# Kernel tuning notes

Measured on AMD Instinct MI355X. Metric: run time of the kernel, lower is better.

Reference implementation:

```python
import jax, jax.numpy as jnp
import numpy as np

NEG_SLOPE = 0.2  # PyG GATConv default negative_slope
N_NODES = 40000
N_EDGES = 640000
IN_DIM = 128
SAT_DIM = 64
HID = 128
OUT_DIM = 54


def gat_conv(x, edge_index, W, a_src, a_dst, bias):
    """PyG GATConv with heads=1, concat=True, add_self_loops=True."""
    n = x.shape[0]
    loops = jnp.arange(n, dtype=edge_index.dtype)
    src = jnp.concatenate([edge_index[0], loops])  # message sources j
    dst = jnp.concatenate([edge_index[1], loops])  # message targets i
    h = x @ W.T                                    # [N, C]
    alpha_s = h @ a_src                            # [N]
    alpha_d = h @ a_dst                            # [N]
    e = jax.nn.leaky_relu(alpha_s[src] + alpha_d[dst], NEG_SLOPE)  # [E]
    # segment softmax over incoming edges of each dst node (self-loops guarantee non-empty segments)
    m = jax.ops.segment_max(e, dst, num_segments=n)
    e = jnp.exp(e - m[dst])
    denom = jax.ops.segment_sum(e, dst, num_segments=n)
    alpha = e / (denom[dst] + 1e-16)
    out = jax.ops.segment_sum(alpha[:, None] * h[src], dst, num_segments=n)
    return out + bias


def setup_inputs() -> dict:
    key = jax.random.key(0)
    ks = jax.random.split(key, 16)
    s = lambda d: 1.0 / np.sqrt(d)
    inp = {
        "x": jax.random.normal(ks[0], (N_NODES, IN_DIM), jnp.float32),
        "edge_index": jax.random.randint(ks[1], (2, N_EDGES), 0, N_NODES, jnp.int32),
        "sat_W": jax.random.normal(ks[2], (HID, SAT_DIM), jnp.float32) * s(SAT_DIM),
        "sat_b": jnp.zeros((HID,), jnp.float32),
        "neigh_W": jax.random.normal(ks[3], (HID, IN_DIM - SAT_DIM), jnp.float32) * s(IN_DIM - SAT_DIM),
        "neigh_b": jnp.zeros((HID,), jnp.float32),
        "conv1_W": jax.random.normal(ks[4], (HID, HID), jnp.float32) * s(HID),
        "conv1_asrc": jax.random.normal(ks[5], (HID,), jnp.float32) * s(HID),
        "conv1_adst": jax.random.normal(ks[6], (HID,), jnp.float32) * s(HID),
        "conv1_b": jnp.zeros((HID,), jnp.float32),
        "conv2_W": jax.random.normal(ks[7], (HID, HID), jnp.float32) * s(HID),
        "conv2_asrc": jax.random.normal(ks[8], (HID,), jnp.float32) * s(HID),
        "conv2_adst": jax.random.normal(ks[9], (HID,), jnp.float32) * s(HID),
        "conv2_b": jnp.zeros((HID,), jnp.float32),
        "fc1_W": jax.random.normal(ks[10], (HID, HID), jnp.float32) * s(HID),
        "fc1_b": jnp.zeros((HID,), jnp.float32),
        "fc2_W": jax.random.normal(ks[11], (OUT_DIM, HID), jnp.float32) * s(HID),
        "fc2_b": jnp.zeros((OUT_DIM,), jnp.float32),
    }
    return inp


def reference(x, edge_index, sat_W, sat_b, neigh_W, neigh_b,
              conv1_W, conv1_asrc, conv1_adst, conv1_b,
              conv2_W, conv2_asrc, conv2_adst, conv2_b,
              fc1_W, fc1_b, fc2_W, fc2_b):
    sat = jax.nn.relu(x[:, :SAT_DIM] @ sat_W.T + sat_b)
    nei = jax.nn.relu(x[:, SAT_DIM:] @ neigh_W.T + neigh_b)
    h = sat + 0.5 * nei
    h = jax.nn.relu(gat_conv(h, edge_index, conv1_W, conv1_asrc, conv1_adst, conv1_b))
    h = jax.nn.relu(gat_conv(h, edge_index, conv2_W, conv2_asrc, conv2_adst, conv2_b))
    h = jax.nn.relu(h @ fc1_W.T + fc1_b)
    return h @ fc2_W.T + fc2_b
```

## Files before the change

### kernel.cpp

```cpp
#include <hip/hip_runtime.h>


#define N_NODES 40000
#define N_EDGES 640000
#define DIM     128

typedef unsigned short u16;
typedef __attribute__((ext_vector_type(8))) short bf16x8;
typedef __attribute__((ext_vector_type(4))) float f32x4;

#define GLOAD_LDS16(GSRC, LDST)                                                \
    __builtin_amdgcn_global_load_lds(                                          \
        (const __attribute__((address_space(1))) void*)(GSRC),                 \
        (__attribute__((address_space(3))) void*)(LDST), 16, 0, 0)

__device__ __forceinline__ u16 f2bf(float v) {
    unsigned u = __float_as_uint(v);
    u += 0x7FFFu + ((u >> 16) & 1u);
    return (u16)(u >> 16);
}
__device__ __forceinline__ float bf2f(u16 h) { return __uint_as_float(((unsigned)h) << 16); }
__device__ __forceinline__ float rdlane_f(float v, int l) {
    return __uint_as_float(__builtin_amdgcn_readlane(__float_as_uint(v), l));
}

__device__ __forceinline__ int hswz(int row, int col) {
    return row * 128 + ((((col >> 2) ^ (row & 7))) << 2) + (col & 3);
}
__device__ __forceinline__ float4 hread4(const float* hbuf, int row, int k) {
    int b = (k >> 2) ^ (row & 7);
    return *(const float4*)&hbuf[row * 128 + (b << 2)];
}
__device__ __forceinline__ void split8(const float* vv, bf16x8& hi, bf16x8& lo) {
#pragma unroll
    for (int i = 0; i < 8; ++i) {
        u16 h = f2bf(vv[i]);
        hi[i] = (short)h;
        lo[i] = (short)f2bf(vv[i] - bf2f(h));
    }
}

#define MFMA3(ACC, AH, AL, BH, BL)                                             \
    ACC = __builtin_amdgcn_mfma_f32_16x16x32_bf16(AH, BH, ACC, 0, 0, 0);       \
    ACC = __builtin_amdgcn_mfma_f32_16x16x32_bf16(AH, BL, ACC, 0, 0, 0);       \
    ACC = __builtin_amdgcn_mfma_f32_16x16x32_bf16(AL, BH, ACC, 0, 0, 0);

__global__ __launch_bounds__(256) void k_wcvt(
    const float* __restrict__ satW, const float* __restrict__ neiW,
    const float* __restrict__ c1W, const float* __restrict__ c2W,
    const float* __restrict__ f1W, const float* __restrict__ f2W,
    u16* __restrict__ wa, int* __restrict__ deg, int* __restrict__ counter) {
    int gid = (blockIdx.y * gridDim.x + blockIdx.x) * 256 + threadIdx.x;
    if (gid < N_NODES) deg[gid] = 1;
    if (gid == 0) *counter = 0;

    int m = blockIdx.y;
    const float* src; int C, K, Cp; int offH, offL;
    switch (m) {
        case 0: src = satW; C = 128; K = 64;  Cp = 128; offH = 0;      offL = 8192;   break;
        case 1: src = neiW; C = 128; K = 64;  Cp = 128; offH = 16384;  offL = 24576;  break;
        case 2: src = c1W;  C = 128; K = 128; Cp = 128; offH = 32768;  offL = 49152;  break;
        case 3: src = c2W;  C = 128; K = 128; Cp = 128; offH = 65536;  offL = 81920;  break;
        case 4: src = f1W;  C = 128; K = 128; Cp = 128; offH = 98304;  offL = 114688; break;
        default:src = f2W;  C = 54;  K = 128; Cp = 64;  offH = 131072; offL = 139264; break;
    }
    int e = blockIdx.x * 256 + threadIdx.x;
    if (e >= Cp * K) return;
    int c = e / K, k = e - c * K;
    float v = (c < C) ? src[c * K + k] : 0.f;
    u16 h = f2bf(v);
    wa[offH + e] = h;
    wa[offL + e] = f2bf(v - bf2f(h));
}

__global__ void k_deg_count(const int* __restrict__ dst, int* __restrict__ deg) {
    int t = blockIdx.x * 256 + threadIdx.x;
    if (t < N_EDGES) atomicAdd(&deg[dst[t]], 1);
}
__global__ void k_assign(const int* __restrict__ deg, int* __restrict__ counter,
                         int* __restrict__ start, int* __restrict__ cursor,
                         int* __restrict__ csr_src) {
    int i = blockIdx.x * 256 + threadIdx.x;
    if (i >= N_NODES) return;
    int d = deg[i];
    int s = atomicAdd(counter, d);
    start[i] = s;
    csr_src[s] = i;
    cursor[i] = s + 1;
}
__global__ void k_fill_edges(const int* __restrict__ src, const int* __restrict__ dst,
                             int* __restrict__ cursor, int* __restrict__ csr_src) {
    int t = blockIdx.x * 256 + threadIdx.x;
    if (t < N_EDGES) {
        int p = atomicAdd(&cursor[dst[t]], 1);
        csr_src[p] = src[t];
    }
}

template<int CT>
__device__ __forceinline__ void stage_W(u16* Ws, const u16* __restrict__ Wh,
                                        const u16* __restrict__ Wl, int kc, int tid) {
    for (int idx = tid; idx < CT * 2 * 2 * 64; idx += 256) {
        int l = idx & 63;
        int q = idx >> 6;
        int hilo = q & 1;
        int ks = (q >> 1) & 1;
        int ct = q >> 2;
        int c = ct * 16 + (l & 15);
        int k = kc * 64 + ks * 32 + (l >> 4) * 8;
        const u16* Wp = hilo ? Wl : Wh;
        GLOAD_LDS16(Wp + (size_t)c * 128 + k, &Ws[idx * 8]);
    }
}
__device__ __forceinline__ void stage_W64(u16* Ws, const u16* __restrict__ Wh,
                                          const u16* __restrict__ Wl, int tid) {
    for (int idx = tid; idx < 2048; idx += 256) {
        int l = idx & 63;
        int q = idx >> 6;
        int hilo = q & 1;
        int ks = (q >> 1) & 1;
        int ct = q >> 2;
        int c = ct * 16 + (l & 15);
        int k = ks * 32 + (l >> 4) * 8;
        const u16* Wp = hilo ? Wl : Wh;
        GLOAD_LDS16(Wp + (size_t)c * 64 + k, &Ws[idx * 8]);
    }
}

__device__ __forceinline__ void alpha_epi(const f32x4* acc, int lane, int r0,
                                          const float* __restrict__ a_src,
                                          const float* __restrict__ a_dst,
                                          float* __restrict__ as_, float* __restrict__ ad_) {
    float ps[4] = {0, 0, 0, 0}, pd[4] = {0, 0, 0, 0};
#pragma unroll
    for (int ct = 0; ct < 8; ++ct) {
        float asv = a_src[ct * 16 + (lane & 15)];
        float adv = a_dst[ct * 16 + (lane & 15)];
#pragma unroll
        for (int r = 0; r < 4; ++r) {
            ps[r] = fmaf(acc[ct][r], asv, ps[r]);
            pd[r] = fmaf(acc[ct][r], adv, pd[r]);
        }
    }
#pragma unroll
    for (int off = 1; off < 16; off <<= 1) {
#pragma unroll
        for (int r = 0; r < 4; ++r) {
            ps[r] += __shfl_xor(ps[r], off);
            pd[r] += __shfl_xor(pd[r], off);
        }
    }
    if ((lane & 15) == 0) {
#pragma unroll
        for (int r = 0; r < 4; ++r) {
            int row = r0 + (lane >> 4) * 4 + r;
            as_[row] = ps[r];
            ad_[row] = pd[r];
        }
    }
}

__global__ __launch_bounds__(256) void k_enc_conv1(
    const float* __restrict__ x,
    const u16* __restrict__ sH, const u16* __restrict__ sL,
    const u16* __restrict__ nH, const u16* __restrict__ nL,
    const float* __restrict__ satb, const float* __restrict__ neib,
    const u16* __restrict__ Wh, const u16* __restrict__ Wl,
    const float* __restrict__ a_src, const float* __restrict__ a_dst,
    u16* __restrict__ outG, float* __restrict__ as_, float* __restrict__ ad_)
{
    __shared__ u16 Wbuf[16384];
    float* hbuf = (float*)Wbuf;
    const int tid = threadIdx.x, lane = tid & 63, wv = tid >> 6;
    const int r0 = blockIdx.x * 64 + wv * 16;
    const int arow = r0 + (lane & 15);
    const int kb = (lane >> 4) * 8;

    bf16x8 axh[4], axl[4];
#pragma unroll
    for (int s = 0; s < 4; ++s) {
        const float* p = x + (size_t)arow * 128 + s * 32 + kb;
        float4 a = *(const float4*)p;
        float4 b = *(const float4*)(p + 4);
        float vv[8] = {a.x, a.y, a.z, a.w, b.x, b.y, b.z, b.w};
        split8(vv, axh[s], axl[s]);
    }

    f32x4 accS[8], accN[8];
#pragma unroll
    for (int ct = 0; ct < 8; ++ct) { accS[ct] = (f32x4){0,0,0,0}; accN[ct] = (f32x4){0,0,0,0}; }

#pragma unroll
    for (int mat = 0; mat < 2; ++mat) {
        if (mat) __syncthreads();
        stage_W64(Wbuf, mat ? nH : sH, mat ? nL : sL, tid);
        __syncthreads();
#pragma unroll
        for (int ct = 0; ct < 8; ++ct) {
#pragma unroll
            for (int ks = 0; ks < 2; ++ks) {
                int s = mat * 2 + ks;
                int base = (ct * 2 + ks) * 1024;
                bf16x8 bh = *reinterpret_cast<const bf16x8*>(&Wbuf[base + lane * 8]);
                bf16x8 bl = *reinterpret_cast<const bf16x8*>(&Wbuf[base + 512 + lane * 8]);
                f32x4* ac = mat ? &accN[ct] : &accS[ct];
                MFMA3((*ac), axh[s], axl[s], bh, bl);
            }
        }
    }
    __syncthreads();

#pragma unroll
    for (int ct = 0; ct < 8; ++ct) {
        int c = ct * 16 + (lane & 15);
        float bs = satb[c], bn = neib[c];
#pragma unroll
        for (int r = 0; r < 4; ++r) {
            int rl = wv * 16 + (lane >> 4) * 4 + r;
            float v = fmaxf(accS[ct][r] + bs, 0.f) + 0.5f * fmaxf(accN[ct][r] + bn, 0.f);
            hbuf[hswz(rl, c)] = v;
        }
    }
    __syncthreads();

    bf16x8 ah[4], al[4];
    const int ar = wv * 16 + (lane & 15);
#pragma unroll
    for (int s = 0; s < 4; ++s) {
        int k0 = s * 32 + kb;
        float4 a = hread4(hbuf, ar, k0);
        float4 b = hread4(hbuf, ar, k0 + 4);
        float vv[8] = {a.x, a.y, a.z, a.w, b.x, b.y, b.z, b.w};
        split8(vv, ah[s], al[s]);
    }
    __syncthreads();

    f32x4 acc[8];
#pragma unroll
    for (int ct = 0; ct < 8; ++ct) acc[ct] = (f32x4){0, 0, 0, 0};
#pragma unroll
    for (int kc = 0; kc < 2; ++kc) {
        if (kc) __syncthreads();
        stage_W<8>(Wbuf, Wh, Wl, kc, tid);
        __syncthreads();
#pragma unroll
        for (int ct = 0; ct < 8; ++ct) {
#pragma unroll
            for (int ks = 0; ks < 2; ++ks) {
                int s = kc * 2 + ks;
                int base = (ct * 2 + ks) * 1024;
                bf16x8 bh = *reinterpret_cast<const bf16x8*>(&Wbuf[base + lane * 8]);
                bf16x8 bl = *reinterpret_cast<const bf16x8*>(&Wbuf[base + 512 + lane * 8]);
                MFMA3(acc[ct], ah[s], al[s], bh, bl);
            }
        }
    }

    alpha_epi(acc, lane, r0, a_src, a_dst, as_, ad_);

#pragma unroll
    for (int ct = 0; ct < 8; ++ct) {
        int c = ct * 16 + (lane & 15);
#pragma unroll
        for (int r = 0; r < 4; ++r) {
            int row = r0 + (lane >> 4) * 4 + r;
            outG[(size_t)row * 128 + c] = f2bf(acc[ct][r]);
        }
    }
}

__global__ __launch_bounds__(256) void k_conv_gemm(
    const u16* __restrict__ Ah, const u16* __restrict__ Al,
    const u16* __restrict__ Wh, const u16* __restrict__ Wl,
    const float* __restrict__ a_src, const float* __restrict__ a_dst,
    u16* __restrict__ outG, float* __restrict__ as_, float* __restrict__ ad_)
{
    __shared__ u16 Wbuf[16384];
    const int tid = threadIdx.x, lane = tid & 63, wv = tid >> 6;
    const int r0 = blockIdx.x * 64 + wv * 16;
    const int arow = r0 + (lane & 15);
    const int kb = (lane >> 4) * 8;

    bf16x8 ah[4], al[4];
#pragma unroll
    for (int s = 0; s < 4; ++s) {
        ah[s] = *reinterpret_cast<const bf16x8*>(Ah + (size_t)arow * 128 + s * 32 + kb);
        al[s] = *reinterpret_cast<const bf16x8*>(Al + (size_t)arow * 128 + s * 32 + kb);
    }

    f32x4 acc[8];
#pragma unroll
    for (int ct = 0; ct < 8; ++ct) acc[ct] = (f32x4){0, 0, 0, 0};
#pragma unroll
    for (int kc = 0; kc < 2; ++kc) {
        if (kc) __syncthreads();
        stage_W<8>(Wbuf, Wh, Wl, kc, tid);
        __syncthreads();
#pragma unroll
        for (int ct = 0; ct < 8; ++ct) {
#pragma unroll
            for (int ks = 0; ks < 2; ++ks) {
                int s = kc * 2 + ks;
                int base = (ct * 2 + ks) * 1024;
                bf16x8 bh = *reinterpret_cast<const bf16x8*>(&Wbuf[base + lane * 8]);
                bf16x8 bl = *reinterpret_cast<const bf16x8*>(&Wbuf[base + 512 + lane * 8]);
                MFMA3(acc[ct], ah[s], al[s], bh, bl);
            }
        }
    }

    alpha_epi(acc, lane, r0, a_src, a_dst, as_, ad_);

#pragma unroll
    for (int ct = 0; ct < 8; ++ct) {
        int c = ct * 16 + (lane & 15);
#pragma unroll
        for (int r = 0; r < 4; ++r) {
            int row = r0 + (lane >> 4) * 4 + r;
            outG[(size_t)row * 128 + c] = f2bf(acc[ct][r]);
        }
    }
}

__global__ __launch_bounds__(256) void k_fc12(
    const u16* __restrict__ Ah, const u16* __restrict__ Al,
    const u16* __restrict__ W1h, const u16* __restrict__ W1l, const float* __restrict__ b1,
    const u16* __restrict__ W2h, const u16* __restrict__ W2l, const float* __restrict__ b2,
    float* __restrict__ out)
{
    __shared__ u16 Wbuf[16384];
    float* hbuf = (float*)Wbuf;
    const int tid = threadIdx.x, lane = tid & 63, wv = tid >> 6;
    const int r0 = blockIdx.x * 64 + wv * 16;
    const int arow = r0 + (lane & 15);
    const int kb = (lane >> 4) * 8;

    bf16x8 ah[4], al[4];
#pragma unroll
    for (int s = 0; s < 4; ++s) {
        ah[s] = *reinterpret_cast<const bf16x8*>(Ah + (size_t)arow * 128 + s * 32 + kb);
        al[s] = *reinterpret_cast<const bf16x8*>(Al + (size_t)arow * 128 + s * 32 + kb);
    }

    f32x4 acc[8];
#pragma unroll
    for (int ct = 0; ct < 8; ++ct) acc[ct] = (f32x4){0, 0, 0, 0};
#pragma unroll
    for (int kc = 0; kc < 2; ++kc) {
        if (kc) __syncthreads();
        stage_W<8>(Wbuf, W1h, W1l, kc, tid);
        __syncthreads();
#pragma unroll
        for (int ct = 0; ct < 8; ++ct) {
#pragma unroll
            for (int ks = 0; ks < 2; ++ks) {
                int s = kc * 2 + ks;
                int base = (ct * 2 + ks) * 1024;
                bf16x8 bh = *reinterpret_cast<const bf16x8*>(&Wbuf[base + lane * 8]);
                bf16x8 bl = *reinterpret_cast<const bf16x8*>(&Wbuf[base + 512 + lane * 8]);
                MFMA3(acc[ct], ah[s], al[s], bh, bl);
            }
        }
    }
    __syncthreads();

#pragma unroll
    for (int ct = 0; ct < 8; ++ct) {
        int c = ct * 16 + (lane & 15);
        float bv = b1[c];
#pragma unroll
        for (int r = 0; r < 4; ++r) {
            int rl = wv * 16 + (lane >> 4) * 4 + r;
            hbuf[hswz(rl, c)] = fmaxf(acc[ct][r] + bv, 0.f);
        }
    }
    __syncthreads();

    bf16x8 a2h[4], a2l[4];
    const int ar = wv * 16 + (lane & 15);
#pragma unroll
    for (int s = 0; s < 4; ++s) {
        int k0 = s * 32 + kb;
        float4 a = hread4(hbuf, ar, k0);
        float4 b = hread4(hbuf, ar, k0 + 4);
        float vv[8] = {a.x, a.y, a.z, a.w, b.x, b.y, b.z, b.w};
        split8(vv, a2h[s], a2l[s]);
    }
    __syncthreads();

    f32x4 acc2[4];
#pragma unroll
    for (int ct = 0; ct < 4; ++ct) acc2[ct] = (f32x4){0, 0, 0, 0};
#pragma unroll
    for (int kc = 0; kc < 2; ++kc) {
        if (kc) __syncthreads();
        stage_W<4>(Wbuf, W2h, W2l, kc, tid);
        __syncthreads();
#pragma unroll
        for (int ct = 0; ct < 4; ++ct) {
#pragma unroll
            for (int ks = 0; ks < 2; ++ks) {
                int s = kc * 2 + ks;
                int base = (ct * 2 + ks) * 1024;
                bf16x8 bh = *reinterpret_cast<const bf16x8*>(&Wbuf[base + lane * 8]);
                bf16x8 bl = *reinterpret_cast<const bf16x8*>(&Wbuf[base + 512 + lane * 8]);
                MFMA3(acc2[ct], a2h[s], a2l[s], bh, bl);
            }
        }
    }

#pragma unroll
    for (int ct = 0; ct < 4; ++ct) {
        int c = ct * 16 + (lane & 15);
#pragma unroll
        for (int r = 0; r < 4; ++r) {
            int row = r0 + (lane >> 4) * 4 + r;
            if (c < 54) out[(size_t)row * 54 + c] = acc2[ct][r] + b2[c];
        }
    }
}

#define DO_PAIRS(NP, TB)                                                      \
    {                                                                         \
        float pw[NP]; const ushort4* hp[NP];                                  \
        _Pragma("unroll")                                                     \
        for (int q = 0; q < NP; ++q) {                                        \
            int e0 = (TB) + 2 * q;                                            \
            float plo = rdlane_f(p, e0), phi = rdlane_f(p, e0 + 1);           \
            int jlo = __builtin_amdgcn_readlane(jj, e0);                      \
            int jhi = __builtin_amdgcn_readlane(jj, e0 + 1);                  \
            pw[q] = hodd ? phi : plo;                                         \
            int j = hodd ? jhi : jlo;                                         \
            hp[q] = (const ushort4*)&hg[(size_t)j * 128 + 4 * l32];           \
        }                                                                     \
        ushort4 hv[NP];                                                       \
        _Pragma("unroll") for (int q = 0; q < NP; ++q) hv[q] = *hp[q];        \
        _Pragma("unroll") for (int q = 0; q < NP; ++q) {                      \
            acc.x = fmaf(pw[q], bf2f(hv[q].x), acc.x);                        \
            acc.y = fmaf(pw[q], bf2f(hv[q].y), acc.y);                        \
            acc.z = fmaf(pw[q], bf2f(hv[q].z), acc.z);                        \
            acc.w = fmaf(pw[q], bf2f(hv[q].w), acc.w);                        \
        }                                                                     \
    }

__global__ __launch_bounds__(256) void k_aggregate(
    const u16* __restrict__ hg, const float* __restrict__ as_,
    const float* __restrict__ ad_, const int* __restrict__ start,
    const int* __restrict__ deg, const int* __restrict__ csr_src,
    const float* __restrict__ bias, u16* __restrict__ outH, u16* __restrict__ outL)
{
    int wid = (blockIdx.x * 256 + threadIdx.x) >> 6;
    int lane = threadIdx.x & 63;
    if (wid >= N_NODES) return;

    const int s0 = start[wid];
    const int s1 = s0 + deg[wid];
    const float adi = ad_[wid];
    const int l32 = lane & 31;
    const bool hodd = lane >= 32;

    float4 acc = make_float4(0.f, 0.f, 0.f, 0.f);
    float ssum = 0.f;
    for (int base = s0; base < s1; base += 64) {
        int k = base + lane;
        int cnt = min(64, s1 - base);
        int jj = 0;
        float p = 0.f;
        if (k < s1) {
            jj = csr_src[k];
            float e = as_[jj] + adi;
            e = (e > 0.f) ? e : 0.2f * e;
            p = __expf(e);
            ssum += p;
        }
        int t = 0;
        for (; t + 16 <= cnt; t += 16) DO_PAIRS(8, t)
        if (t + 8 <= cnt) { DO_PAIRS(4, t) t += 8; }
        if (t + 4 <= cnt) { DO_PAIRS(2, t) t += 4; }
        for (; t < cnt; t += 2) DO_PAIRS(1, t)
    }
#pragma unroll
    for (int off = 32; off; off >>= 1) ssum += __shfl_xor(ssum, off);
    acc.x += __shfl_xor(acc.x, 32);
    acc.y += __shfl_xor(acc.y, 32);
    acc.z += __shfl_xor(acc.z, 32);
    acc.w += __shfl_xor(acc.w, 32);
    float inv = 1.f / (ssum + 1e-16f);

    if (!hodd) {
        float4 bv = *(const float4*)&bias[4 * l32];
        float o0 = fmaxf(fmaf(acc.x, inv, bv.x), 0.f);
        float o1 = fmaxf(fmaf(acc.y, inv, bv.y), 0.f);
        float o2 = fmaxf(fmaf(acc.z, inv, bv.z), 0.f);
        float o3 = fmaxf(fmaf(acc.w, inv, bv.w), 0.f);
        u16 h0 = f2bf(o0), h1 = f2bf(o1), h2 = f2bf(o2), h3 = f2bf(o3);
        ushort4 hvv = make_ushort4(h0, h1, h2, h3);
        ushort4 lvv = make_ushort4(f2bf(o0 - bf2f(h0)), f2bf(o1 - bf2f(h1)),
                                   f2bf(o2 - bf2f(h2)), f2bf(o3 - bf2f(h3)));
        *(ushort4*)&outH[(size_t)wid * 128 + 4 * l32] = hvv;
        *(ushort4*)&outL[(size_t)wid * 128 + 4 * l32] = lvv;
    }
}

extern "C" void kernel_launch(void* const* d_in, const int* in_sizes, int n_in,
                              void* d_out, int out_size, void* d_ws, size_t ws_size,
                              hipStream_t stream) {
    (void)in_sizes; (void)n_in; (void)out_size; (void)ws_size;

    const float* x       = (const float*)d_in[0];
    const int*   ei      = (const int*)d_in[1];
    const float* sat_W   = (const float*)d_in[2];
    const float* sat_b   = (const float*)d_in[3];
    const float* neigh_W = (const float*)d_in[4];
    const float* neigh_b = (const float*)d_in[5];
    const float* c1_W    = (const float*)d_in[6];
    const float* c1_as   = (const float*)d_in[7];
    const float* c1_ad   = (const float*)d_in[8];
    const float* c1_b    = (const float*)d_in[9];
    const float* c2_W    = (const float*)d_in[10];
    const float* c2_as   = (const float*)d_in[11];
    const float* c2_ad   = (const float*)d_in[12];
    const float* c2_b    = (const float*)d_in[13];
    const float* fc1_W   = (const float*)d_in[14];
    const float* fc1_b   = (const float*)d_in[15];
    const float* fc2_W   = (const float*)d_in[16];
    const float* fc2_b   = (const float*)d_in[17];

    const int* e_src = ei;
    const int* e_dst = ei + N_EDGES;

    char* w = (char*)d_ws;
    u16*   hG     = (u16*)  (w);
    u16*   hH     = (u16*)  (w + 10240000);
    u16*   hL     = (u16*)  (w + 20480000);
    float* as_    = (float*)(w + 30720000);
    float* ad_    = (float*)(w + 30880000);
    int*   deg    = (int*)  (w + 31040000);
    int*   start  = (int*)  (w + 31200000);
    int*   cursor = (int*)  (w + 31360000);
    int*   counter= (int*)  (w + 31520000);
    int*   csr    = (int*)  (w + 31520256);
    u16*   wa     = (u16*)  (w + 34240256);

    u16 *satH = wa,          *satL = wa + 8192;
    u16 *neiH = wa + 16384,  *neiL = wa + 24576;
    u16 *c1H  = wa + 32768,  *c1L  = wa + 49152;
    u16 *c2H  = wa + 65536,  *c2L  = wa + 81920;
    u16 *f1H  = wa + 98304,  *f1L  = wa + 114688;
    u16 *f2H  = wa + 131072, *f2L  = wa + 139264;

    dim3 b(256);
    k_wcvt<<<dim3(64, 6), b, 0, stream>>>(sat_W, neigh_W, c1_W, c2_W, fc1_W, fc2_W,
                                          wa, deg, counter);
    k_deg_count <<<2500, b, 0, stream>>>(e_dst, deg);
    k_assign    <<<157,  b, 0, stream>>>(deg, counter, start, cursor, csr);
    k_fill_edges<<<2500, b, 0, stream>>>(e_src, e_dst, cursor, csr);

    k_enc_conv1<<<625, b, 0, stream>>>(x, satH, satL, neiH, neiL, sat_b, neigh_b,
                                       c1H, c1L, c1_as, c1_ad, hG, as_, ad_);
    k_aggregate<<<10000, b, 0, stream>>>(hG, as_, ad_, start, deg, csr, c1_b, hH, hL);

    k_conv_gemm<<<625, b, 0, stream>>>(hH, hL, c2H, c2L, c2_as, c2_ad, hG, as_, ad_);
    k_aggregate<<<10000, b, 0, stream>>>(hG, as_, ad_, start, deg, csr, c2_b, hH, hL);

    k_fc12<<<625, b, 0, stream>>>(hH, hL, f1H, f1L, fc1_b, f2H, f2L, fc2_b,
                                  (float*)d_out);
}
```

Measured before the change: 199.5 us.

## Split gathered features into per-XCD column chunks for L2-local aggregation

The GEMM kernels now write node features in four column-chunked planes of 32 bf16 each instead of row-major 128-wide rows. The aggregate kernel is launched with four times as many blocks, and each block's XCD index (blockIdx & 7) picks which chunk it gathers. The intent is that each XCD's L2 only ever caches one quarter of the feature table, which should raise the gather hit rate. In exchange, each wave processes 4 edges per step with 4-byte loads and redoes the softmax weight computation once per chunk, and correctness relies on the round-robin block-to-XCD mapping.

```diff
diff --git a/kernel.cpp b/kernel.cpp
--- a/kernel.cpp
+++ b/kernel.cpp
@@ -4,6 +4,7 @@
 #define N_NODES 40000
 #define N_EDGES 640000
 #define DIM     128
+#define CHSTRIDE ((size_t)N_NODES * 32)
 
 typedef unsigned short u16;
 typedef __attribute__((ext_vector_type(8))) short bf16x8;
@@ -44,6 +45,8 @@
     ACC = __builtin_amdgcn_mfma_f32_16x16x32_bf16(AH, BH, ACC, 0, 0, 0);       \
     ACC = __builtin_amdgcn_mfma_f32_16x16x32_bf16(AH, BL, ACC, 0, 0, 0);       \
     ACC = __builtin_amdgcn_mfma_f32_16x16x32_bf16(AL, BH, ACC, 0, 0, 0);
+
+#define HG_IDX(ROW, C) ((size_t)((C) >> 5) * CHSTRIDE + (size_t)(ROW) * 32 + ((C) & 31))
 
 __global__ __launch_bounds__(256) void k_wcvt(
     const float* __restrict__ satW, const float* __restrict__ neiW,
@@ -264,7 +267,7 @@
 #pragma unroll
         for (int r = 0; r < 4; ++r) {
             int row = r0 + (lane >> 4) * 4 + r;
-            outG[(size_t)row * 128 + c] = f2bf(acc[ct][r]);
+            outG[HG_IDX(row, c)] = f2bf(acc[ct][r]);
         }
     }
 }
@@ -317,7 +320,7 @@
 #pragma unroll
         for (int r = 0; r < 4; ++r) {
             int row = r0 + (lane >> 4) * 4 + r;
-            outG[(size_t)row * 128 + c] = f2bf(acc[ct][r]);
+            outG[HG_IDX(row, c)] = f2bf(acc[ct][r]);
         }
     }
 }
@@ -420,46 +423,50 @@
     }
 }
 
-#define DO_PAIRS(NP, TB)                                                      \
+#define DO_QUADS(NQ, TB)                                                      \
     {                                                                         \
-        float pw[NP]; const ushort4* hp[NP];                                  \
+        float pw[NQ]; const unsigned* hp[NQ];                                 \
         _Pragma("unroll")                                                     \
-        for (int q = 0; q < NP; ++q) {                                        \
-            int e0 = (TB) + 2 * q;                                            \
-            float plo = rdlane_f(p, e0), phi = rdlane_f(p, e0 + 1);           \
-            int jlo = __builtin_amdgcn_readlane(jj, e0);                      \
-            int jhi = __builtin_amdgcn_readlane(jj, e0 + 1);                  \
-            pw[q] = hodd ? phi : plo;                                         \
-            int j = hodd ? jhi : jlo;                                         \
-            hp[q] = (const ushort4*)&hg[(size_t)j * 128 + 4 * l32];           \
+        for (int q = 0; q < NQ; ++q) {                                        \
+            int e0 = (TB) + 4 * q;                                            \
+            float pa = rdlane_f(p, e0),     pb = rdlane_f(p, e0 + 1);         \
+            float pc = rdlane_f(p, e0 + 2), pe = rdlane_f(p, e0 + 3);         \
+            int ja = __builtin_amdgcn_readlane(jj, e0);                       \
+            int jb = __builtin_amdgcn_readlane(jj, e0 + 1);                   \
+            int jc = __builtin_amdgcn_readlane(jj, e0 + 2);                   \
+            int je = __builtin_amdgcn_readlane(jj, e0 + 3);                   \
+            pw[q]  = esel == 0 ? pa : (esel == 1 ? pb : (esel == 2 ? pc : pe));\
+            int j  = esel == 0 ? ja : (esel == 1 ? jb : (esel == 2 ? jc : je));\
+            hp[q] = (const unsigned*)&hc[(size_t)j * 32 + 2 * dp];            \
         }                                                                     \
-        ushort4 hv[NP];                                                       \
-        _Pragma("unroll") for (int q = 0; q < NP; ++q) hv[q] = *hp[q];        \
-        _Pragma("unroll") for (int q = 0; q < NP; ++q) {                      \
-            acc.x = fmaf(pw[q], bf2f(hv[q].x), acc.x);                        \
-            acc.y = fmaf(pw[q], bf2f(hv[q].y), acc.y);                        \
-            acc.z = fmaf(pw[q], bf2f(hv[q].z), acc.z);                        \
-            acc.w = fmaf(pw[q], bf2f(hv[q].w), acc.w);                        \
+        unsigned hv[NQ];                                                      \
+        _Pragma("unroll") for (int q = 0; q < NQ; ++q) hv[q] = *hp[q];        \
+        _Pragma("unroll") for (int q = 0; q < NQ; ++q) {                      \
+            acc.x = fmaf(pw[q], bf2f((u16)(hv[q] & 0xffffu)), acc.x);         \
+            acc.y = fmaf(pw[q], bf2f((u16)(hv[q] >> 16)), acc.y);             \
         }                                                                     \
     }
 
 __global__ __launch_bounds__(256) void k_aggregate(
-    const u16* __restrict__ hg, const float* __restrict__ as_,
+    const u16* __restrict__ hgc, const float* __restrict__ as_,
     const float* __restrict__ ad_, const int* __restrict__ start,
     const int* __restrict__ deg, const int* __restrict__ csr_src,
     const float* __restrict__ bias, u16* __restrict__ outH, u16* __restrict__ outL)
 {
-    int wid = (blockIdx.x * 256 + threadIdx.x) >> 6;
-    int lane = threadIdx.x & 63;
-    if (wid >= N_NODES) return;
+    const int bid = blockIdx.x;
+    const int wv = threadIdx.x >> 6;
+    const int lane = threadIdx.x & 63;
+    const int xcd = bid & 7;
+    const int chunk = xcd >> 1;
+    const int wid = ((bid >> 3) * 2 + (xcd & 1)) * 4 + wv;
+    const u16* hc = hgc + (size_t)chunk * CHSTRIDE;
 
     const int s0 = start[wid];
     const int s1 = s0 + deg[wid];
     const float adi = ad_[wid];
-    const int l32 = lane & 31;
-    const bool hodd = lane >= 32;
-
-    float4 acc = make_float4(0.f, 0.f, 0.f, 0.f);
+    const int esel = lane >> 4, dp = lane & 15;
+
+    float2 acc = make_float2(0.f, 0.f);
     float ssum = 0.f;
     for (int base = s0; base < s1; base += 64) {
         int k = base + lane;
@@ -474,31 +481,27 @@
             ssum += p;
         }
         int t = 0;
-        for (; t + 16 <= cnt; t += 16) DO_PAIRS(8, t)
-        if (t + 8 <= cnt) { DO_PAIRS(4, t) t += 8; }
-        if (t + 4 <= cnt) { DO_PAIRS(2, t) t += 4; }
-        for (; t < cnt; t += 2) DO_PAIRS(1, t)
+        for (; t + 16 <= cnt; t += 16) DO_QUADS(4, t)
+        if (t + 8 <= cnt) { DO_QUADS(2, t) t += 8; }
+        for (; t < cnt; t += 4) DO_QUADS(1, t)
     }
 #pragma unroll
     for (int off = 32; off; off >>= 1) ssum += __shfl_xor(ssum, off);
+    acc.x += __shfl_xor(acc.x, 16);
+    acc.y += __shfl_xor(acc.y, 16);
     acc.x += __shfl_xor(acc.x, 32);
     acc.y += __shfl_xor(acc.y, 32);
-    acc.z += __shfl_xor(acc.z, 32);
-    acc.w += __shfl_xor(acc.w, 32);
     float inv = 1.f / (ssum + 1e-16f);
 
-    if (!hodd) {
-        float4 bv = *(const float4*)&bias[4 * l32];
+    if (lane < 16) {
+        float2 bv = *(const float2*)&bias[chunk * 32 + 2 * dp];
         float o0 = fmaxf(fmaf(acc.x, inv, bv.x), 0.f);
         float o1 = fmaxf(fmaf(acc.y, inv, bv.y), 0.f);
-        float o2 = fmaxf(fmaf(acc.z, inv, bv.z), 0.f);
-        float o3 = fmaxf(fmaf(acc.w, inv, bv.w), 0.f);
-        u16 h0 = f2bf(o0), h1 = f2bf(o1), h2 = f2bf(o2), h3 = f2bf(o3);
-        ushort4 hvv = make_ushort4(h0, h1, h2, h3);
-        ushort4 lvv = make_ushort4(f2bf(o0 - bf2f(h0)), f2bf(o1 - bf2f(h1)),
-                                   f2bf(o2 - bf2f(h2)), f2bf(o3 - bf2f(h3)));
-        *(ushort4*)&outH[(size_t)wid * 128 + 4 * l32] = hvv;
-        *(ushort4*)&outL[(size_t)wid * 128 + 4 * l32] = lvv;
+        u16 h0 = f2bf(o0), h1 = f2bf(o1);
+        unsigned hw = (unsigned)h0 | ((unsigned)h1 << 16);
+        unsigned lw = (unsigned)f2bf(o0 - bf2f(h0)) | ((unsigned)f2bf(o1 - bf2f(h1)) << 16);
+        *(unsigned*)&outH[(size_t)wid * 128 + chunk * 32 + 2 * dp] = hw;
+        *(unsigned*)&outL[(size_t)wid * 128 + chunk * 32 + 2 * dp] = lw;
     }
 }
 
@@ -558,10 +561,10 @@
 
     k_enc_conv1<<<625, b, 0, stream>>>(x, satH, satL, neiH, neiL, sat_b, neigh_b,
                                        c1H, c1L, c1_as, c1_ad, hG, as_, ad_);
-    k_aggregate<<<10000, b, 0, stream>>>(hG, as_, ad_, start, deg, csr, c1_b, hH, hL);
+    k_aggregate<<<40000, b, 0, stream>>>(hG, as_, ad_, start, deg, csr, c1_b, hH, hL);
 
     k_conv_gemm<<<625, b, 0, stream>>>(hH, hL, c2H, c2L, c2_as, c2_ad, hG, as_, ad_);
-    k_aggregate<<<10000, b, 0, stream>>>(hG, as_, ad_, start, deg, csr, c2_b, hH, hL);
+    k_aggregate<<<40000, b, 0, stream>>>(hG, as_, ad_, start, deg, csr, c2_b, hH, hL);
 
     k_fc12<<<625, b, 0, stream>>>(hH, hL, f1H, f1L, fc1_b, f2H, f2L, fc2_b,
                                   (float*)d_out);
```

New measurement: 285.6 us. 43.2% more time.

## Double-buffer weight staging in LDS to overlap loads and cut barriers

Applied to the files above, without the earlier changes.

Each GEMM kernel gets a second 32KB shared buffer so weight chunks can be staged ahead, prefetched at kernel start alongside the activation loads, which removes several barrier-separated stage/compute rounds. In k_conv_gemm both K-halves are staged up front and consumed in a single pass. LDS per block doubles to 64KB, which can lower occupancy (fewer resident blocks per CU) and may offset the saved latency.

```diff
diff --git a/kernel.cpp b/kernel.cpp
--- a/kernel.cpp
+++ b/kernel.cpp
@@ -169,12 +169,16 @@
     const float* __restrict__ a_src, const float* __restrict__ a_dst,
     u16* __restrict__ outG, float* __restrict__ as_, float* __restrict__ ad_)
 {
-    __shared__ u16 Wbuf[16384];
-    float* hbuf = (float*)Wbuf;
+    __shared__ u16 WbufA[16384];
+    __shared__ u16 WbufB[16384];
+    float* hbuf = (float*)WbufA;
     const int tid = threadIdx.x, lane = tid & 63, wv = tid >> 6;
     const int r0 = blockIdx.x * 64 + wv * 16;
     const int arow = r0 + (lane & 15);
     const int kb = (lane >> 4) * 8;
+
+    stage_W<8>(WbufB, Wh, Wl, 0, tid);
+    stage_W64(WbufA, sH, sL, tid);
 
     bf16x8 axh[4], axl[4];
 #pragma unroll
@@ -190,22 +194,28 @@
 #pragma unroll
     for (int ct = 0; ct < 8; ++ct) { accS[ct] = (f32x4){0,0,0,0}; accN[ct] = (f32x4){0,0,0,0}; }
 
-#pragma unroll
-    for (int mat = 0; mat < 2; ++mat) {
-        if (mat) __syncthreads();
-        stage_W64(Wbuf, mat ? nH : sH, mat ? nL : sL, tid);
-        __syncthreads();
-#pragma unroll
-        for (int ct = 0; ct < 8; ++ct) {
-#pragma unroll
-            for (int ks = 0; ks < 2; ++ks) {
-                int s = mat * 2 + ks;
-                int base = (ct * 2 + ks) * 1024;
-                bf16x8 bh = *reinterpret_cast<const bf16x8*>(&Wbuf[base + lane * 8]);
-                bf16x8 bl = *reinterpret_cast<const bf16x8*>(&Wbuf[base + 512 + lane * 8]);
-                f32x4* ac = mat ? &accN[ct] : &accS[ct];
-                MFMA3((*ac), axh[s], axl[s], bh, bl);
-            }
+    __syncthreads();
+#pragma unroll
+    for (int ct = 0; ct < 8; ++ct) {
+#pragma unroll
+        for (int ks = 0; ks < 2; ++ks) {
+            int base = (ct * 2 + ks) * 1024;
+            bf16x8 bh = *reinterpret_cast<const bf16x8*>(&WbufA[base + lane * 8]);
+            bf16x8 bl = *reinterpret_cast<const bf16x8*>(&WbufA[base + 512 + lane * 8]);
+            MFMA3(accS[ct], axh[ks], axl[ks], bh, bl);
+        }
+    }
+    __syncthreads();
+    stage_W64(WbufA, nH, nL, tid);
+    __syncthreads();
+#pragma unroll
+    for (int ct = 0; ct < 8; ++ct) {
+#pragma unroll
+        for (int ks = 0; ks < 2; ++ks) {
+            int base = (ct * 2 + ks) * 1024;
+            bf16x8 bh = *reinterpret_cast<const bf16x8*>(&WbufA[base + lane * 8]);
+            bf16x8 bl = *reinterpret_cast<const bf16x8*>(&WbufA[base + 512 + lane * 8]);
+            MFMA3(accN[ct], axh[ks + 2], axl[ks + 2], bh, bl);
         }
     }
     __syncthreads();
@@ -235,24 +245,30 @@
     }
     __syncthreads();
 
+    stage_W<8>(WbufA, Wh, Wl, 1, tid);
+
     f32x4 acc[8];
 #pragma unroll
     for (int ct = 0; ct < 8; ++ct) acc[ct] = (f32x4){0, 0, 0, 0};
 #pragma unroll
-    for (int kc = 0; kc < 2; ++kc) {
-        if (kc) __syncthreads();
-        stage_W<8>(Wbuf, Wh, Wl, kc, tid);
-        __syncthreads();
-#pragma unroll
-        for (int ct = 0; ct < 8; ++ct) {
-#pragma unroll
-            for (int ks = 0; ks < 2; ++ks) {
-                int s = kc * 2 + ks;
-                int base = (ct * 2 + ks) * 1024;
-                bf16x8 bh = *reinterpret_cast<const bf16x8*>(&Wbuf[base + lane * 8]);
-                bf16x8 bl = *reinterpret_cast<const bf16x8*>(&Wbuf[base + 512 + lane * 8]);
-                MFMA3(acc[ct], ah[s], al[s], bh, bl);
-            }
+    for (int ct = 0; ct < 8; ++ct) {
+#pragma unroll
+        for (int ks = 0; ks < 2; ++ks) {
+            int base = (ct * 2 + ks) * 1024;
+            bf16x8 bh = *reinterpret_cast<const bf16x8*>(&WbufB[base + lane * 8]);
+            bf16x8 bl = *reinterpret_cast<const bf16x8*>(&WbufB[base + 512 + lane * 8]);
+            MFMA3(acc[ct], ah[ks], al[ks], bh, bl);
+        }
+    }
+    __syncthreads();
+#pragma unroll
+    for (int ct = 0; ct < 8; ++ct) {
+#pragma unroll
+        for (int ks = 0; ks < 2; ++ks) {
+            int base = (ct * 2 + ks) * 1024;
+            bf16x8 bh = *reinterpret_cast<const bf16x8*>(&WbufA[base + lane * 8]);
+            bf16x8 bl = *reinterpret_cast<const bf16x8*>(&WbufA[base + 512 + lane * 8]);
+            MFMA3(acc[ct], ah[2 + ks], al[2 + ks], bh, bl);
         }
     }
 
@@ -275,12 +291,16 @@
     const float* __restrict__ a_src, const float* __restrict__ a_dst,
     u16* __restrict__ outG, float* __restrict__ as_, float* __restrict__ ad_)
 {
-    __shared__ u16 Wbuf[16384];
+    __shared__ u16 WbufA[16384];
+    __shared__ u16 WbufB[16384];
     const int tid = threadIdx.x, lane = tid & 63, wv = tid >> 6;
     const int r0 = blockIdx.x * 64 + wv * 16;
     const int arow = r0 + (lane & 15);
     const int kb = (lane >> 4) * 8;
 
+    stage_W<8>(WbufA, Wh, Wl, 0, tid);
+    stage_W<8>(WbufB, Wh, Wl, 1, tid);
+
     bf16x8 ah[4], al[4];
 #pragma unroll
     for (int s = 0; s < 4; ++s) {
@@ -291,21 +311,19 @@
     f32x4 acc[8];
 #pragma unroll
     for (int ct = 0; ct < 8; ++ct) acc[ct] = (f32x4){0, 0, 0, 0};
-#pragma unroll
-    for (int kc = 0; kc < 2; ++kc) {
-        if (kc) __syncthreads();
-        stage_W<8>(Wbuf, Wh, Wl, kc, tid);
-        __syncthreads();
-#pragma unroll
-        for (int ct = 0; ct < 8; ++ct) {
-#pragma unroll
-            for (int ks = 0; ks < 2; ++ks) {
-                int s = kc * 2 + ks;
-                int base = (ct * 2 + ks) * 1024;
-                bf16x8 bh = *reinterpret_cast<const bf16x8*>(&Wbuf[base + lane * 8]);
-                bf16x8 bl = *reinterpret_cast<const bf16x8*>(&Wbuf[base + 512 + lane * 8]);
-                MFMA3(acc[ct], ah[s], al[s], bh, bl);
-            }
+
+    __syncthreads();
+#pragma unroll
+    for (int ct = 0; ct < 8; ++ct) {
+#pragma unroll
+        for (int ks = 0; ks < 2; ++ks) {
+            int base = (ct * 2 + ks) * 1024;
+            bf16x8 bh = *reinterpret_cast<const bf16x8*>(&WbufA[base + lane * 8]);
+            bf16x8 bl = *reinterpret_cast<const bf16x8*>(&WbufA[base + 512 + lane * 8]);
+            MFMA3(acc[ct], ah[ks], al[ks], bh, bl);
+            bf16x8 ch = *reinterpret_cast<const bf16x8*>(&WbufB[base + lane * 8]);
+            bf16x8 cl = *reinterpret_cast<const bf16x8*>(&WbufB[base + 512 + lane * 8]);
+            MFMA3(acc[ct], ah[2 + ks], al[2 + ks], ch, cl);
         }
     }
 
@@ -328,13 +346,18 @@
     const u16* __restrict__ W2h, const u16* __restrict__ W2l, const float* __restrict__ b2,
     float* __restrict__ out)
 {
-    __shared__ u16 Wbuf[16384];
-    float* hbuf = (float*)Wbuf;
+    __shared__ u16 WbufA[16384];
+    __shared__ u16 WbufB[16384];
+    float* hbuf = (float*)WbufA;
     const int tid = threadIdx.x, lane = tid & 63, wv = tid >> 6;
     const int r0 = blockIdx.x * 64 + wv * 16;
     const int arow = r0 + (lane & 15);
     const int kb = (lane >> 4) * 8;
 
+    stage_W<4>(WbufB, W2h, W2l, 0, tid);
+    stage_W<4>(WbufB + 8192, W2h, W2l, 1, tid);
+    stage_W<8>(WbufA, W1h, W1l, 0, tid);
+
     bf16x8 ah[4], al[4];
 #pragma unroll
     for (int s = 0; s < 4; ++s) {
@@ -345,21 +368,29 @@
     f32x4 acc[8];
 #pragma unroll
     for (int ct = 0; ct < 8; ++ct) acc[ct] = (f32x4){0, 0, 0, 0};
-#pragma unroll
-    for (int kc = 0; kc < 2; ++kc) {
-        if (kc) __syncthreads();
-        stage_W<8>(Wbuf, W1h, W1l, kc, tid);
-        __syncthreads();
-#pragma unroll
-        for (int ct = 0; ct < 8; ++ct) {
-#pragma unroll
-            for (int ks = 0; ks < 2; ++ks) {
-                int s = kc * 2 + ks;
-                int base = (ct * 2 + ks) * 1024;
-                bf16x8 bh = *reinterpret_cast<const bf16x8*>(&Wbuf[base + lane * 8]);
-                bf16x8 bl = *reinterpret_cast<const bf16x8*>(&Wbuf[base + 512 + lane * 8]);
-                MFMA3(acc[ct], ah[s], al[s], bh, bl);
-            }
+
+    __syncthreads();
+#pragma unroll
+    for (int ct = 0; ct < 8; ++ct) {
+#pragma unroll
+        for (int ks = 0; ks < 2; ++ks) {
+            int base = (ct * 2 + ks) * 1024;
+            bf16x8 bh = *reinterpret_cast<const bf16x8*>(&WbufA[base + lane * 8]);
+            bf16x8 bl = *reinterpret_cast<const bf16x8*>(&WbufA[base + 512 + lane * 8]);
+            MFMA3(acc[ct], ah[ks], al[ks], bh, bl);
+        }
+    }
+    __syncthreads();
+    stage_W<8>(WbufA, W1h, W1l, 1, tid);
+    __syncthreads();
+#pragma unroll
+    for (int ct = 0; ct < 8; ++ct) {
+#pragma unroll
+        for (int ks = 0; ks < 2; ++ks) {
+            int base = (ct * 2 + ks) * 1024;
+            bf16x8 bh = *reinterpret_cast<const bf16x8*>(&WbufA[base + lane * 8]);
+            bf16x8 bl = *reinterpret_cast<const bf16x8*>(&WbufA[base + 512 + lane * 8]);
+            MFMA3(acc[ct], ah[2 + ks], al[2 + ks], bh, bl);
         }
     }
     __syncthreads();
@@ -386,24 +417,21 @@
         float vv[8] = {a.x, a.y, a.z, a.w, b.x, b.y, b.z, b.w};
         split8(vv, a2h[s], a2l[s]);
     }
-    __syncthreads();
 
     f32x4 acc2[4];
 #pragma unroll
     for (int ct = 0; ct < 4; ++ct) acc2[ct] = (f32x4){0, 0, 0, 0};
 #pragma unroll
     for (int kc = 0; kc < 2; ++kc) {
-        if (kc) __syncthreads();
-        stage_W<4>(Wbuf, W2h, W2l, kc, tid);
-        __syncthreads();
+        const u16* Wb = WbufB + kc * 8192;
 #pragma unroll
         for (int ct = 0; ct < 4; ++ct) {
 #pragma unroll
             for (int ks = 0; ks < 2; ++ks) {
                 int s = kc * 2 + ks;
                 int base = (ct * 2 + ks) * 1024;
-                bf16x8 bh = *reinterpret_cast<const bf16x8*>(&Wbuf[base + lane * 8]);
-                bf16x8 bl = *reinterpret_cast<const bf16x8*>(&Wbuf[base + 512 + lane * 8]);
+                bf16x8 bh = *reinterpret_cast<const bf16x8*>(&Wb[base + lane * 8]);
+                bf16x8 bl = *reinterpret_cast<const bf16x8*>(&Wb[base + 512 + lane * 8]);
                 MFMA3(acc2[ct], a2h[s], a2l[s], bh, bl);
             }
         }
```

Result: slower. 205.2 us (+2.8%).
